# Kernel optimization log

Hardware: AMD Instinct MI355X
Metric: run time of the kernel (lower is better)

The kernel has to match this reference:

```python
import jax, jax.numpy as jnp
import numpy as np

B, L, K, H = 4, 256, 256, 768
KEY_SIZE, VAL_SIZE = 50000, 10000


def setup_inputs() -> dict:
    key = jax.random.key(0)
    k1, k2, k3, k4, k5, k6 = jax.random.split(key, 6)
    return {
        "hidden_state": jax.random.normal(k1, (B, L, H), dtype=jnp.float32),
        "key_seq": jax.random.randint(k2, (B, K), 0, KEY_SIZE),
        "value_matrix": jax.random.randint(k3, (B, L, K), 0, VAL_SIZE),
        "key_mask_matrix": jax.random.randint(k4, (B, L, K), 0, 2),
        "key_emb_table": jax.random.normal(k5, (KEY_SIZE, H), dtype=jnp.float32),
        "val_emb_table": jax.random.normal(k6, (VAL_SIZE, H), dtype=jnp.float32),
    }


def reference(hidden_state, key_seq, value_matrix, key_mask_matrix,
              key_emb_table, val_emb_table):
    temper = jnp.asarray(H, jnp.float32) ** 0.5
    # embedding lookups
    embedding_key = key_emb_table[key_seq]            # [B, K, H]
    embedding_val = val_emb_table[value_matrix]       # [B, L, K, H]
    # scores: hidden [B,L,H] x key [B,K,H] -> [B,L,K]
    u = jnp.einsum('blh,bkh->blk', hidden_state, embedding_key) / temper
    mask = jnp.clip(key_mask_matrix, 0, 1).astype(jnp.float32)
    delta_exp_u = jnp.exp(u) * mask                   # masked exp
    sum_delta = jnp.sum(delta_exp_u, axis=2, keepdims=True)
    p = delta_exp_u / (sum_delta + 1e-10)             # masked softmax [B,L,K]
    # weighted value sum (avoids the original's [H,B,L,K] broadcast+permute)
    o = jnp.einsum('blk,blkh->blh', p, embedding_val)
    return o + hidden_state
```

## Files before the change

kernel.cpp:

```cpp
#include <hip/hip_runtime.h>
#include <math.h>

typedef float    f32x2 __attribute__((ext_vector_type(2)));
typedef float    f32x4 __attribute__((ext_vector_type(4)));
typedef _Float16 f16x2 __attribute__((ext_vector_type(2)));

static constexpr int B_ = 4;
static constexpr int L_ = 256;
static constexpr int K_ = 256;
static constexpr int H_ = 768;
static constexpr int H2_ = H_ / 2;
static constexpr int VAL_SIZE_ = 10000;
static constexpr float INV_TEMPER = 0.03608439182435161f;

__device__ __forceinline__ unsigned pack_f16x2(float a, float b) {
  f16x2 p = {(_Float16)a, (_Float16)b};
  return __builtin_bit_cast(unsigned, p);
}
__device__ __forceinline__ float fdot2u(unsigned a, unsigned b, float c) {
#if __has_builtin(__builtin_amdgcn_fdot2)
  return __builtin_amdgcn_fdot2(__builtin_bit_cast(f16x2, a),
                                __builtin_bit_cast(f16x2, b), c, false);
#else
  f16x2 va = __builtin_bit_cast(f16x2, a);
  f16x2 vb = __builtin_bit_cast(f16x2, b);
  return c + (float)va.x * (float)vb.x + (float)va.y * (float)vb.y;
#endif
}

__device__ __forceinline__ float4 nt_load4(const float* p) {
  f32x4 v = __builtin_nontemporal_load(reinterpret_cast<const f32x4*>(p));
  return make_float4(v.x, v.y, v.z, v.w);
}

#if __has_builtin(__builtin_amdgcn_cvt_pk_fp8_f32)
#define HW_FP8_ENC 1
#endif
#if __has_builtin(__builtin_amdgcn_cvt_pk_f32_fp8)
#define HW_FP8_DEC 1
#endif

__device__ __forceinline__ unsigned fp8_enc1(float f) {
  unsigned s = (__float_as_uint(f) >> 31) << 7;
  float af = fminf(fabsf(f), 448.0f);
  unsigned em;
  if (af < 0.015625f) {
    em = (unsigned)rintf(af * 512.0f);
  } else {
    unsigned m = __float_as_uint(af);
    m += 0x7ffffu + ((m >> 20) & 1u);
    em = (m >> 20) - (120u << 3);
  }
  return s | em;
}
__device__ __forceinline__ float fp8_dec1(unsigned b) {
  unsigned em = b & 0x7fu;
  unsigned sbit = (b & 0x80u) << 24;
  float n = __uint_as_float(sbit | ((em + 960u) << 20));
  float sub = __uint_as_float(sbit | 0x3F800000u) * (float)em * 0.001953125f;
  return em >= 8u ? n : sub;
}
__device__ __forceinline__ unsigned fp8_enc4(float a, float b, float c, float d) {
#ifdef HW_FP8_ENC
  int w = 0;
  w = __builtin_amdgcn_cvt_pk_fp8_f32(a, b, w, false);
  w = __builtin_amdgcn_cvt_pk_fp8_f32(c, d, w, true);
  return (unsigned)w;
#else
  return fp8_enc1(a) | (fp8_enc1(b) << 8) | (fp8_enc1(c) << 16) | (fp8_enc1(d) << 24);
#endif
}
__device__ __forceinline__ void fp8_dec4(unsigned w, float* o) {
#ifdef HW_FP8_DEC
  f32x2 lo = __builtin_amdgcn_cvt_pk_f32_fp8((int)w, false);
  f32x2 hi = __builtin_amdgcn_cvt_pk_f32_fp8((int)w, true);
  o[0] = lo.x; o[1] = lo.y; o[2] = hi.x; o[3] = hi.y;
#else
  o[0] = fp8_dec1(w & 0xffu);
  o[1] = fp8_dec1((w >> 8) & 0xffu);
  o[2] = fp8_dec1((w >> 16) & 0xffu);
  o[3] = fp8_dec1(w >> 24);
#endif
}

static constexpr int TBLK = (K_ / 64) * (H_ / 64) * B_;
static constexpr int SBLK = (L_ / 4) * B_;
static constexpr int CBLK = (VAL_SIZE_ * H_) / 4096;

__global__ __launch_bounds__(256)
void k_gather_keys_T(const int* __restrict__ key_seq,
                     const float* __restrict__ key_emb,
                     unsigned* __restrict__ ET2) {
  __shared__ float tile[64][65];
  const int blk  = blockIdx.x;
  const int kb   = (blk % (K_ / 64)) * 64;
  const int hb   = ((blk / (K_ / 64)) % (H_ / 64)) * 64;
  const int b    = blk / ((K_ / 64) * (H_ / 64));
  const int t    = threadIdx.x;
  const int sub  = t >> 6;
  const int lane = t & 63;

#pragma unroll
  for (int p = 0; p < 16; ++p) {
    const int kl  = p * 4 + sub;
    const int row = key_seq[b * K_ + kb + kl];
    tile[kl][lane] = key_emb[(size_t)row * H_ + hb + lane];
  }
  __syncthreads();
#pragma unroll
  for (int p = 0; p < 8; ++p) {
    const int hl2 = p * 4 + sub;
    ET2[((size_t)b * H2_ + (hb >> 1) + hl2) * K_ + kb + lane] =
        pack_f16x2(tile[lane][2 * hl2], tile[lane][2 * hl2 + 1]);
  }
}

__global__ __launch_bounds__(256)
void k_scores_convert(const float* __restrict__ hidden,
                      const unsigned* __restrict__ ET2,
                      const int* __restrict__ mask,
                      const float* __restrict__ vtab,
                      float* __restrict__ P,
                      unsigned char* __restrict__ VT8) {
  __shared__ unsigned hid2[4 * H2_];
  __shared__ float4   part[4][256];
  const int t = threadIdx.x;

  if (blockIdx.x >= SBLK) {
    const size_t base = (size_t)(blockIdx.x - SBLK) * 4096;
#pragma unroll
    for (int c = 0; c < 4; ++c) {
      const size_t e0 = base + (size_t)c * 1024 + (size_t)t * 4;
      const float4 a = nt_load4(vtab + e0);
      *reinterpret_cast<unsigned*>(VT8 + e0) = fp8_enc4(a.x, a.y, a.z, a.w);
    }
    return;
  }

  const int l0 = (blockIdx.x % (L_ / 4)) * 4;
  const int b  = blockIdx.x / (L_ / 4);

  const float* hsrc = hidden + ((size_t)b * L_ + l0) * H_;
  for (int i = t; i < 4 * H2_; i += 256) {
    const float2 hv = *reinterpret_cast<const float2*>(hsrc + 2 * i);
    hid2[i] = pack_f16x2(hv.x, hv.y);
  }
  __syncthreads();

  const int kq = t & 63;
  const int hq = t >> 6;

  float4 acc[4];
#pragma unroll
  for (int l = 0; l < 4; ++l) acc[l] = make_float4(0.f, 0.f, 0.f, 0.f);

  const unsigned* etp =
      ET2 + (size_t)b * H2_ * K_ + (size_t)(hq * 96) * K_ + kq * 4;
  const int hbase2 = hq * 96;
#pragma unroll 4
  for (int hh = 0; hh < 96; ++hh) {
    const uint4 e = *reinterpret_cast<const uint4*>(etp + (size_t)hh * K_);
#pragma unroll
    for (int l = 0; l < 4; ++l) {
      const unsigned hv2 = hid2[l * H2_ + hbase2 + hh];
      acc[l].x = fdot2u(e.x, hv2, acc[l].x);
      acc[l].y = fdot2u(e.y, hv2, acc[l].y);
      acc[l].z = fdot2u(e.z, hv2, acc[l].z);
      acc[l].w = fdot2u(e.w, hv2, acc[l].w);
    }
  }
#pragma unroll
  for (int l = 0; l < 4; ++l) part[l][t] = acc[l];
  __syncthreads();

  const int kq2 = t & 63;
  const int l2  = t >> 6;
  float4 a = part[l2][kq2];
  const float4 b1 = part[l2][64 + kq2];
  const float4 c  = part[l2][128 + kq2];
  const float4 d  = part[l2][192 + kq2];
  a.x += b1.x + c.x + d.x;
  a.y += b1.y + c.y + d.y;
  a.z += b1.z + c.z + d.z;
  a.w += b1.w + c.w + d.w;

  const int lrow = l0 + l2;
  const int4 m4 = *reinterpret_cast<const int4*>(
      mask + ((size_t)b * L_ + lrow) * K_ + kq2 * 4);
  float4 ex;
  ex.x = (m4.x > 0) ? expf(a.x * INV_TEMPER) : 0.f;
  ex.y = (m4.y > 0) ? expf(a.y * INV_TEMPER) : 0.f;
  ex.z = (m4.z > 0) ? expf(a.z * INV_TEMPER) : 0.f;
  ex.w = (m4.w > 0) ? expf(a.w * INV_TEMPER) : 0.f;

  float s = ex.x + ex.y + ex.z + ex.w;
#pragma unroll
  for (int off = 32; off > 0; off >>= 1) s += __shfl_down(s, off);
  const float tot = __shfl(s, 0) + 1e-10f;

  float4 p4;
  p4.x = ex.x / tot;
  p4.y = ex.y / tot;
  p4.z = ex.z / tot;
  p4.w = ex.w / tot;
  *reinterpret_cast<float4*>(P + ((size_t)b * L_ + lrow) * K_ + kq2 * 4) = p4;
}

__global__ __launch_bounds__(384)
void k_pv_add(const float* __restrict__ hidden,
              const int* __restrict__ vmat,
              const float* __restrict__ P,
              const unsigned char* __restrict__ VT8,
              float* __restrict__ out) {
  __shared__ float pw[K_];
  __shared__ int   vidx[K_];
  __shared__ int   wcounts[4];
  __shared__ float osum[3][H_];

  const int l = blockIdx.x;
  const int b = blockIdx.y;
  const int t = threadIdx.x;
  const int lane = t & 63;
  const int wid  = t >> 6;
  const size_t rowoff = ((size_t)b * L_ + l) * K_;

  float pval = 0.f;
  bool pred = false;
  unsigned long long mball = 0;
  if (t < K_) {
    pval = P[rowoff + t];
    pred = (pval != 0.f);
    mball = __ballot(pred);
    if (lane == 0) wcounts[wid] = (int)__popcll(mball);
  }
  __syncthreads();
  const int n = wcounts[0] + wcounts[1] + wcounts[2] + wcounts[3];
  if (t < K_ && pred) {
    int base = 0;
#pragma unroll
    for (int w = 0; w < 4; ++w)
      if (w < wid) base += wcounts[w];
    const int pos = base + (int)__popcll(mball & ((1ull << lane) - 1ull));
    pw[pos]   = pval;
    vidx[pos] = vmat[rowoff + t];
  }
  __syncthreads();

  const int slice = t / 96;
  const int g     = t % 96;

  float acc[8];
#pragma unroll
  for (int i = 0; i < 8; ++i) acc[i] = 0.f;

#pragma unroll 4
  for (int j = slice; j < n; j += 4) {
    const float w = pw[j];
    const uint2 v = *reinterpret_cast<const uint2*>(
        VT8 + (size_t)vidx[j] * H_ + g * 8);
    float f[8];
    fp8_dec4(v.x, f);
    fp8_dec4(v.y, f + 4);
#pragma unroll
    for (int i = 0; i < 8; ++i) acc[i] += w * f[i];
  }

  if (slice < 3) {
    *reinterpret_cast<float4*>(&osum[slice][g * 8]) =
        make_float4(acc[0], acc[1], acc[2], acc[3]);
    *reinterpret_cast<float4*>(&osum[slice][g * 8 + 4]) =
        make_float4(acc[4], acc[5], acc[6], acc[7]);
  }
  __syncthreads();
  if (slice == 3) {
    const float* hrow = hidden + ((size_t)b * L_ + l) * H_ + g * 8;
    const float4 h0 = *reinterpret_cast<const float4*>(hrow);
    const float4 h1 = *reinterpret_cast<const float4*>(hrow + 4);
    float r[8];
#pragma unroll
    for (int i = 0; i < 8; ++i) {
      float sum = acc[i];
#pragma unroll
      for (int s = 0; s < 3; ++s) sum += osum[s][g * 8 + i];
      r[i] = sum;
    }
    float4 r0 = make_float4(r[0] + h0.x, r[1] + h0.y, r[2] + h0.z, r[3] + h0.w);
    float4 r1 = make_float4(r[4] + h1.x, r[5] + h1.y, r[6] + h1.z, r[7] + h1.w);
    float* orow = out + ((size_t)b * L_ + l) * H_ + g * 8;
    *reinterpret_cast<float4*>(orow)     = r0;
    *reinterpret_cast<float4*>(orow + 4) = r1;
  }
}

extern "C" void kernel_launch(void* const* d_in, const int* in_sizes, int n_in,
                              void* d_out, int out_size, void* d_ws, size_t ws_size,
                              hipStream_t stream) {
  (void)in_sizes; (void)n_in; (void)out_size; (void)ws_size;
  const float* hidden  = (const float*)d_in[0];
  const int*   key_seq = (const int*)d_in[1];
  const int*   vmat    = (const int*)d_in[2];
  const int*   mask    = (const int*)d_in[3];
  const float* key_emb = (const float*)d_in[4];
  const float* val_emb = (const float*)d_in[5];
  float* out = (float*)d_out;

  unsigned char* VT8 = (unsigned char*)d_ws;
  unsigned*      ET2 = (unsigned*)(VT8 + (size_t)VAL_SIZE_ * H_);
  float*         P   = (float*)(ET2 + (size_t)B_ * H2_ * K_);

  k_gather_keys_T<<<TBLK, 256, 0, stream>>>(key_seq, key_emb, ET2);
  k_scores_convert<<<SBLK + CBLK, 256, 0, stream>>>(hidden, ET2, mask,
                                                    val_emb, P, VT8);
  k_pv_add<<<dim3(L_, B_), 384, 0, stream>>>(hidden, vmat, P, VT8, out);
}
```

Baseline: 39.19 us.

## Fuse score softmax with PV accumulation and move value-table conversion into prep

Moves the FP8 value-table conversion into the key-gather kernel and fuses the scores/softmax kernel with the PV-weighted sum, so each 4-row block compacts nonzero probabilities in shared memory and accumulates the value rows directly. This removes one launch and the global round-trip of the probability matrix P. The tradeoff is fewer blocks for the PV phase (256 blocks of 512 threads instead of 1024 blocks), heavier shared memory use per block, and idle threads during the scores phase.

```diff
diff --git a/kernel.cpp b/kernel.cpp
--- a/kernel.cpp
+++ b/kernel.cpp
@@ -88,15 +88,29 @@
 static constexpr int CBLK = (VAL_SIZE_ * H_) / 4096;
 
 __global__ __launch_bounds__(256)
-void k_gather_keys_T(const int* __restrict__ key_seq,
-                     const float* __restrict__ key_emb,
-                     unsigned* __restrict__ ET2) {
+void k_prep(const int* __restrict__ key_seq,
+            const float* __restrict__ key_emb,
+            const float* __restrict__ vtab,
+            unsigned* __restrict__ ET2,
+            unsigned char* __restrict__ VT8) {
   __shared__ float tile[64][65];
+  const int t = threadIdx.x;
+
+  if (blockIdx.x >= TBLK) {
+    const size_t base = (size_t)(blockIdx.x - TBLK) * 4096;
+#pragma unroll
+    for (int c = 0; c < 4; ++c) {
+      const size_t e0 = base + (size_t)c * 1024 + (size_t)t * 4;
+      const float4 a = nt_load4(vtab + e0);
+      *reinterpret_cast<unsigned*>(VT8 + e0) = fp8_enc4(a.x, a.y, a.z, a.w);
+    }
+    return;
+  }
+
   const int blk  = blockIdx.x;
   const int kb   = (blk % (K_ / 64)) * 64;
   const int hb   = ((blk / (K_ / 64)) % (H_ / 64)) * 64;
   const int b    = blk / ((K_ / 64) * (H_ / 64));
-  const int t    = threadIdx.x;
   const int sub  = t >> 6;
   const int lane = t & 63;
 
@@ -115,180 +129,162 @@
   }
 }
 
-__global__ __launch_bounds__(256)
-void k_scores_convert(const float* __restrict__ hidden,
-                      const unsigned* __restrict__ ET2,
-                      const int* __restrict__ mask,
-                      const float* __restrict__ vtab,
-                      float* __restrict__ P,
-                      unsigned char* __restrict__ VT8) {
+__global__ __launch_bounds__(512)
+void k_scores_pv(const float* __restrict__ hidden,
+                 const unsigned* __restrict__ ET2,
+                 const int* __restrict__ mask,
+                 const int* __restrict__ vmat,
+                 const unsigned char* __restrict__ VT8,
+                 float* __restrict__ out) {
   __shared__ unsigned hid2[4 * H2_];
   __shared__ float4   part[4][256];
-  const int t = threadIdx.x;
-
-  if (blockIdx.x >= SBLK) {
-    const size_t base = (size_t)(blockIdx.x - SBLK) * 4096;
-#pragma unroll
-    for (int c = 0; c < 4; ++c) {
-      const size_t e0 = base + (size_t)c * 1024 + (size_t)t * 4;
-      const float4 a = nt_load4(vtab + e0);
-      *reinterpret_cast<unsigned*>(VT8 + e0) = fp8_enc4(a.x, a.y, a.z, a.w);
-    }
-    return;
-  }
-
-  const int l0 = (blockIdx.x % (L_ / 4)) * 4;
-  const int b  = blockIdx.x / (L_ / 4);
+  __shared__ int      vmat_lds[4][K_];
+  __shared__ float    pw[4][K_];
+  __shared__ int      vidx[4][K_];
+  __shared__ float    osum[4][H_];
+  __shared__ int      nrow[4];
+
+  const int t  = threadIdx.x;
+  const int l0 = (blockIdx.x & 63) * 4;
+  const int b  = blockIdx.x >> 6;
 
   const float* hsrc = hidden + ((size_t)b * L_ + l0) * H_;
-  for (int i = t; i < 4 * H2_; i += 256) {
+  for (int i = t; i < 4 * H2_; i += 512) {
     const float2 hv = *reinterpret_cast<const float2*>(hsrc + 2 * i);
     hid2[i] = pack_f16x2(hv.x, hv.y);
   }
-  __syncthreads();
-
-  const int kq = t & 63;
-  const int hq = t >> 6;
-
-  float4 acc[4];
-#pragma unroll
-  for (int l = 0; l < 4; ++l) acc[l] = make_float4(0.f, 0.f, 0.f, 0.f);
-
-  const unsigned* etp =
-      ET2 + (size_t)b * H2_ * K_ + (size_t)(hq * 96) * K_ + kq * 4;
-  const int hbase2 = hq * 96;
+  if (t >= 256) {
+    const int i  = t - 256;
+    const int r  = i >> 6;
+    const int c4 = (i & 63) * 4;
+    *reinterpret_cast<int4*>(&vmat_lds[r][c4]) =
+        *reinterpret_cast<const int4*>(vmat + ((size_t)b * L_ + l0 + r) * K_ + c4);
+  }
+  __syncthreads();
+
+  if (t < 256) {
+    const int kq = t & 63;
+    const int hq = t >> 6;
+    float4 acc[4];
+#pragma unroll
+    for (int l = 0; l < 4; ++l) acc[l] = make_float4(0.f, 0.f, 0.f, 0.f);
+
+    const unsigned* etp =
+        ET2 + (size_t)b * H2_ * K_ + (size_t)(hq * 96) * K_ + kq * 4;
+    const int hbase2 = hq * 96;
 #pragma unroll 4
-  for (int hh = 0; hh < 96; ++hh) {
-    const uint4 e = *reinterpret_cast<const uint4*>(etp + (size_t)hh * K_);
-#pragma unroll
-    for (int l = 0; l < 4; ++l) {
-      const unsigned hv2 = hid2[l * H2_ + hbase2 + hh];
-      acc[l].x = fdot2u(e.x, hv2, acc[l].x);
-      acc[l].y = fdot2u(e.y, hv2, acc[l].y);
-      acc[l].z = fdot2u(e.z, hv2, acc[l].z);
-      acc[l].w = fdot2u(e.w, hv2, acc[l].w);
-    }
-  }
-#pragma unroll
-  for (int l = 0; l < 4; ++l) part[l][t] = acc[l];
-  __syncthreads();
-
-  const int kq2 = t & 63;
-  const int l2  = t >> 6;
-  float4 a = part[l2][kq2];
-  const float4 b1 = part[l2][64 + kq2];
-  const float4 c  = part[l2][128 + kq2];
-  const float4 d  = part[l2][192 + kq2];
-  a.x += b1.x + c.x + d.x;
-  a.y += b1.y + c.y + d.y;
-  a.z += b1.z + c.z + d.z;
-  a.w += b1.w + c.w + d.w;
-
-  const int lrow = l0 + l2;
-  const int4 m4 = *reinterpret_cast<const int4*>(
-      mask + ((size_t)b * L_ + lrow) * K_ + kq2 * 4);
-  float4 ex;
-  ex.x = (m4.x > 0) ? expf(a.x * INV_TEMPER) : 0.f;
-  ex.y = (m4.y > 0) ? expf(a.y * INV_TEMPER) : 0.f;
-  ex.z = (m4.z > 0) ? expf(a.z * INV_TEMPER) : 0.f;
-  ex.w = (m4.w > 0) ? expf(a.w * INV_TEMPER) : 0.f;
-
-  float s = ex.x + ex.y + ex.z + ex.w;
-#pragma unroll
-  for (int off = 32; off > 0; off >>= 1) s += __shfl_down(s, off);
-  const float tot = __shfl(s, 0) + 1e-10f;
-
-  float4 p4;
-  p4.x = ex.x / tot;
-  p4.y = ex.y / tot;
-  p4.z = ex.z / tot;
-  p4.w = ex.w / tot;
-  *reinterpret_cast<float4*>(P + ((size_t)b * L_ + lrow) * K_ + kq2 * 4) = p4;
-}
-
-__global__ __launch_bounds__(384)
-void k_pv_add(const float* __restrict__ hidden,
-              const int* __restrict__ vmat,
-              const float* __restrict__ P,
-              const unsigned char* __restrict__ VT8,
-              float* __restrict__ out) {
-  __shared__ float pw[K_];
-  __shared__ int   vidx[K_];
-  __shared__ int   wcounts[4];
-  __shared__ float osum[3][H_];
-
-  const int l = blockIdx.x;
-  const int b = blockIdx.y;
-  const int t = threadIdx.x;
+    for (int hh = 0; hh < 96; ++hh) {
+      const uint4 e = *reinterpret_cast<const uint4*>(etp + (size_t)hh * K_);
+#pragma unroll
+      for (int l = 0; l < 4; ++l) {
+        const unsigned hv2 = hid2[l * H2_ + hbase2 + hh];
+        acc[l].x = fdot2u(e.x, hv2, acc[l].x);
+        acc[l].y = fdot2u(e.y, hv2, acc[l].y);
+        acc[l].z = fdot2u(e.z, hv2, acc[l].z);
+        acc[l].w = fdot2u(e.w, hv2, acc[l].w);
+      }
+    }
+#pragma unroll
+    for (int l = 0; l < 4; ++l) part[l][t] = acc[l];
+  }
+  __syncthreads();
+
+  if (t < 256) {
+    const int kq2 = t & 63;
+    const int l2  = t >> 6;
+    float4 a = part[l2][kq2];
+    const float4 b1 = part[l2][64 + kq2];
+    const float4 c  = part[l2][128 + kq2];
+    const float4 d  = part[l2][192 + kq2];
+    a.x += b1.x + c.x + d.x;
+    a.y += b1.y + c.y + d.y;
+    a.z += b1.z + c.z + d.z;
+    a.w += b1.w + c.w + d.w;
+
+    const int lrow = l0 + l2;
+    const int4 m4 = *reinterpret_cast<const int4*>(
+        mask + ((size_t)b * L_ + lrow) * K_ + kq2 * 4);
+    float ex[4];
+    ex[0] = (m4.x > 0) ? expf(a.x * INV_TEMPER) : 0.f;
+    ex[1] = (m4.y > 0) ? expf(a.y * INV_TEMPER) : 0.f;
+    ex[2] = (m4.z > 0) ? expf(a.z * INV_TEMPER) : 0.f;
+    ex[3] = (m4.w > 0) ? expf(a.w * INV_TEMPER) : 0.f;
+
+    float s = ex[0] + ex[1] + ex[2] + ex[3];
+#pragma unroll
+    for (int off = 32; off > 0; off >>= 1) s += __shfl_down(s, off);
+    const float tot = __shfl(s, 0) + 1e-10f;
+    const float rtot = 1.0f / tot;
+
+    const unsigned long long lt = (1ull << kq2) - 1ull;
+    unsigned long long m[4];
+    int run = 0;
+    int pos[4];
+#pragma unroll
+    for (int cc = 0; cc < 4; ++cc) {
+      m[cc] = __ballot(ex[cc] != 0.f);
+      pos[cc] = run + (int)__popcll(m[cc] & lt);
+      run += (int)__popcll(m[cc]);
+    }
+#pragma unroll
+    for (int cc = 0; cc < 4; ++cc) {
+      if (ex[cc] != 0.f) {
+        pw[l2][pos[cc]]   = ex[cc] * rtot;
+        vidx[l2][pos[cc]] = vmat_lds[l2][kq2 * 4 + cc];
+      }
+    }
+    if (kq2 == 0) nrow[l2] = run;
+  }
+  __syncthreads();
+
+  const int w    = t >> 6;
   const int lane = t & 63;
-  const int wid  = t >> 6;
-  const size_t rowoff = ((size_t)b * L_ + l) * K_;
-
-  float pval = 0.f;
-  bool pred = false;
-  unsigned long long mball = 0;
-  if (t < K_) {
-    pval = P[rowoff + t];
-    pred = (pval != 0.f);
-    mball = __ballot(pred);
-    if (lane == 0) wcounts[wid] = (int)__popcll(mball);
-  }
-  __syncthreads();
-  const int n = wcounts[0] + wcounts[1] + wcounts[2] + wcounts[3];
-  if (t < K_ && pred) {
-    int base = 0;
-#pragma unroll
-    for (int w = 0; w < 4; ++w)
-      if (w < wid) base += wcounts[w];
-    const int pos = base + (int)__popcll(mball & ((1ull << lane) - 1ull));
-    pw[pos]   = pval;
-    vidx[pos] = vmat[rowoff + t];
-  }
-  __syncthreads();
-
-  const int slice = t / 96;
-  const int g     = t % 96;
-
-  float acc[8];
-#pragma unroll
-  for (int i = 0; i < 8; ++i) acc[i] = 0.f;
+  const int r    = w & 3;
+  const int half = w >> 2;
+  const int n    = nrow[r];
+
+  float acc[12];
+#pragma unroll
+  for (int i = 0; i < 12; ++i) acc[i] = 0.f;
 
 #pragma unroll 4
-  for (int j = slice; j < n; j += 4) {
-    const float w = pw[j];
-    const uint2 v = *reinterpret_cast<const uint2*>(
-        VT8 + (size_t)vidx[j] * H_ + g * 8);
-    float f[8];
+  for (int j = half; j < n; j += 2) {
+    const float wgt = pw[r][j];
+    const int   idx = vidx[r][j];
+    const uint3 v = *reinterpret_cast<const uint3*>(
+        VT8 + (size_t)idx * H_ + lane * 12);
+    float f[12];
     fp8_dec4(v.x, f);
     fp8_dec4(v.y, f + 4);
-#pragma unroll
-    for (int i = 0; i < 8; ++i) acc[i] += w * f[i];
-  }
-
-  if (slice < 3) {
-    *reinterpret_cast<float4*>(&osum[slice][g * 8]) =
-        make_float4(acc[0], acc[1], acc[2], acc[3]);
-    *reinterpret_cast<float4*>(&osum[slice][g * 8 + 4]) =
-        make_float4(acc[4], acc[5], acc[6], acc[7]);
-  }
-  __syncthreads();
-  if (slice == 3) {
-    const float* hrow = hidden + ((size_t)b * L_ + l) * H_ + g * 8;
-    const float4 h0 = *reinterpret_cast<const float4*>(hrow);
-    const float4 h1 = *reinterpret_cast<const float4*>(hrow + 4);
-    float r[8];
-#pragma unroll
-    for (int i = 0; i < 8; ++i) {
-      float sum = acc[i];
-#pragma unroll
-      for (int s = 0; s < 3; ++s) sum += osum[s][g * 8 + i];
-      r[i] = sum;
-    }
-    float4 r0 = make_float4(r[0] + h0.x, r[1] + h0.y, r[2] + h0.z, r[3] + h0.w);
-    float4 r1 = make_float4(r[4] + h1.x, r[5] + h1.y, r[6] + h1.z, r[7] + h1.w);
-    float* orow = out + ((size_t)b * L_ + l) * H_ + g * 8;
-    *reinterpret_cast<float4*>(orow)     = r0;
-    *reinterpret_cast<float4*>(orow + 4) = r1;
+    fp8_dec4(v.z, f + 8);
+#pragma unroll
+    for (int i = 0; i < 12; ++i) acc[i] += wgt * f[i];
+  }
+
+  if (half == 0) {
+#pragma unroll
+    for (int c = 0; c < 3; ++c)
+      *reinterpret_cast<float4*>(&osum[r][lane * 12 + c * 4]) =
+          make_float4(acc[c * 4], acc[c * 4 + 1], acc[c * 4 + 2], acc[c * 4 + 3]);
+  }
+  __syncthreads();
+  if (half == 1) {
+#pragma unroll
+    for (int i = 0; i < 12; ++i) osum[r][lane * 12 + i] += acc[i];
+  }
+  __syncthreads();
+
+  if (half == 1) {
+    const float* hrow = hidden + ((size_t)b * L_ + l0 + r) * H_;
+    float*       orow = out    + ((size_t)b * L_ + l0 + r) * H_;
+#pragma unroll
+    for (int c = 0; c < 3; ++c) {
+      const int h0 = c * 256 + lane * 4;
+      const float4 ov = *reinterpret_cast<const float4*>(&osum[r][h0]);
+      const float4 hv = *reinterpret_cast<const float4*>(hrow + h0);
+      *reinterpret_cast<float4*>(orow + h0) =
+          make_float4(ov.x + hv.x, ov.y + hv.y, ov.z + hv.z, ov.w + hv.w);
+    }
   }
 }
 
@@ -306,10 +302,7 @@
 
   unsigned char* VT8 = (unsigned char*)d_ws;
   unsigned*      ET2 = (unsigned*)(VT8 + (size_t)VAL_SIZE_ * H_);
-  float*         P   = (float*)(ET2 + (size_t)B_ * H2_ * K_);
-
-  k_gather_keys_T<<<TBLK, 256, 0, stream>>>(key_seq, key_emb, ET2);
-  k_scores_convert<<<SBLK + CBLK, 256, 0, stream>>>(hidden, ET2, mask,
-                                                    val_emb, P, VT8);
-  k_pv_add<<<dim3(L_, B_), 384, 0, stream>>>(hidden, vmat, P, VT8, out);
-}
+
+  k_prep<<<TBLK + CBLK, 256, 0, stream>>>(key_seq, key_emb, val_emb, ET2, VT8);
+  k_scores_pv<<<SBLK, 512, 0, stream>>>(hidden, ET2, mask, vmat, VT8, out);
+}
```

After: 39.46 us. Within noise of the previous version (+0.7%).
